# Kernel tuning notes

Hardware: AMD Instinct MI355X
Metric: run time of the kernel (lower is better)

The kernel has to match this reference:

```python
import jax, jax.numpy as jnp
import numpy as np

D = 1024  # input_size == context_size

def setup_inputs() -> dict:
    key = jax.random.key(0)
    ks = jax.random.split(key, 8)
    B, S = 16, 4096
    s = 1.0 / np.sqrt(D)
    return {
        "x": jax.random.normal(ks[0], (B, S, D), dtype=jnp.float32),
        "context": jax.random.normal(ks[1], (B, D), dtype=jnp.float32),
        "W_in": jax.random.uniform(ks[2], (D, D), jnp.float32, -s, s),
        "b_in": jax.random.uniform(ks[3], (D,), jnp.float32, -s, s),
        "W_ctx": jax.random.uniform(ks[4], (D, D), jnp.float32, -s, s),
        "b_ctx": jax.random.uniform(ks[5], (D,), jnp.float32, -s, s),
        "w_att": jax.random.uniform(ks[6], (D,), jnp.float32, -s, s),
        "b_att": jax.random.uniform(ks[7], (), jnp.float32, -s, s),
    }

def reference(x, context, W_in, b_in, W_ctx, b_ctx, w_att, b_att):
    # projected_input: [B,S,D]; projected_context: [B,D] broadcast over S
    pi = jnp.einsum('bsd,ed->bse', x, W_in) + b_in
    pc = jnp.einsum('bd,ed->be', context, W_ctx) + b_ctx
    h = jnp.tanh(pi + pc[:, None, :])                      # [B,S,D]
    scores = jnp.einsum('bsd,d->bs', h, w_att) + b_att      # [B,S]
    weights = jax.nn.softmax(scores, axis=1)                # [B,S]
    context_vector = jnp.einsum('bs,bsd->bd', weights, x)   # [B,D]
    # dropout is identity in eval mode
    return context_vector
```

## Files before the change

kernel.cpp:

```cpp
#include <hip/hip_runtime.h>
#include <hip/hip_bf16.h>
#include <math.h>

#define NB 16
#define NS 4096
#define ND 1024
#define NM (NB * NS)

#define WS_T       0
#define WS_SCORES  16384
#define WS_WEIGHTS (WS_SCORES + NB * NS)
#define WS_SHARED  (WS_WEIGHTS + NB * NS)
#define WS_XBF16   (WS_SHARED + 524288)
#define WS_SPART   (WS_XBF16 + 33554432)
#define WS_NEED    (((size_t)WS_SPART + 524288) * 4)

typedef short v8s __attribute__((ext_vector_type(8)));
typedef float v4f __attribute__((ext_vector_type(4)));
typedef unsigned short ushort;

#define G_AS __attribute__((address_space(1)))
#define L_AS __attribute__((address_space(3)))

__device__ __forceinline__ ushort f2bf(float f) {
    __hip_bfloat16 h = __float2bfloat16(f);
    return *reinterpret_cast<ushort*>(&h);
}

__device__ __forceinline__ float bf2f(ushort u) {
    return __uint_as_float(((unsigned)u) << 16);
}

__device__ __forceinline__ float fast_tanh(float x) {
    float e = __expf(2.0f * x);
    return 1.0f - 2.0f / (e + 1.0f);
}

__global__ __launch_bounds__(256) void convw_kernel(const float* __restrict__ W,
                                                    ushort* __restrict__ Wb) {
    int flat = blockIdx.x * 256 + threadIdx.x;
#pragma unroll
    for (int j = 0; j < 2; ++j) {
        int idx = flat + j * 131072;
        float4 v = ((const float4*)W)[idx];
        ushort4 o;
        o.x = f2bf(v.x); o.y = f2bf(v.y); o.z = f2bf(v.z); o.w = f2bf(v.w);
        ((ushort4*)Wb)[idx] = o;
    }
}

__global__ __launch_bounds__(256) void convx_kernel(const float* __restrict__ x,
                                                    ushort* __restrict__ xb) {
    size_t base = (size_t)blockIdx.x * 256 + threadIdx.x;
#pragma unroll
    for (int i = 0; i < 16; ++i) {
        size_t idx8 = base + (size_t)i * 524288;
        float4 a = ((const float4*)x)[idx8 * 2];
        float4 c = ((const float4*)x)[idx8 * 2 + 1];
        v8s o;
        o[0] = (short)f2bf(a.x); o[1] = (short)f2bf(a.y);
        o[2] = (short)f2bf(a.z); o[3] = (short)f2bf(a.w);
        o[4] = (short)f2bf(c.x); o[5] = (short)f2bf(c.y);
        o[6] = (short)f2bf(c.z); o[7] = (short)f2bf(c.w);
        ((v8s*)xb)[idx8] = o;
    }
}

__global__ __launch_bounds__(256) void tvec_kernel(const float* __restrict__ context,
                                                   const float* __restrict__ W_ctx,
                                                   const float* __restrict__ b_in,
                                                   const float* __restrict__ b_ctx,
                                                   float* __restrict__ t) {
    __shared__ float ctx[ND];
    int b = blockIdx.y;
    int tid = threadIdx.x;
    for (int i = tid; i < ND; i += 256) ctx[i] = context[b * ND + i];
    __syncthreads();
    int e = blockIdx.x * 64 + (tid >> 2);
    int kq = tid & 3;
    const float4* wr = (const float4*)(W_ctx + (size_t)e * ND + kq * 256);
    const float4* cr = (const float4*)(ctx + kq * 256);
    float acc = 0.f;
#pragma unroll 4
    for (int k = 0; k < 64; ++k) {
        float4 w = wr[k];
        float4 c = cr[k];
        acc += c.x * w.x + c.y * w.y + c.z * w.z + c.w * w.w;
    }
    acc += __shfl_xor(acc, 1);
    acc += __shfl_xor(acc, 2);
    if (kq == 0) t[b * ND + e] = acc + b_in[e] + b_ctx[e];
}

__global__ __launch_bounds__(256, 4) void scores_tile_kernel(const ushort* __restrict__ xbf,
                                                             const ushort* __restrict__ Wb,
                                                             const float* __restrict__ t,
                                                             const float* __restrict__ w_att,
                                                             float* __restrict__ spart) {
    __shared__ ushort As[2][4096];
    __shared__ ushort Bs[2][4096];
    __shared__ float red[4][64];

    int tid = threadIdx.x;
    int o = blockIdx.x;
    int rt = (o & 7) * 64 + (o >> 6);
    int ct = (o >> 3) & 7;
    int row0 = rt << 7;
    int e0 = ct << 7;
    int b = row0 >> 12;

    int g0 = tid, g1 = tid + 256;
    const ushort* gaA0 = xbf + (size_t)(row0 + (g0 >> 2)) * ND + (g0 & 3) * 8;
    const ushort* gaA1 = xbf + (size_t)(row0 + (g1 >> 2)) * ND + (g1 & 3) * 8;
    const ushort* gaB0 = Wb  + (size_t)(e0  + (g0 >> 2)) * ND + (g0 & 3) * 8;
    const ushort* gaB1 = Wb  + (size_t)(e0  + (g1 >> 2)) * ND + (g1 & 3) * 8;

    int w = tid >> 6, l = tid & 63;
    int l15 = l & 15, kq4 = l >> 4;
    int R = (w >> 1) * 64;
    int E = (w & 1) * 64;

    v4f acc[4][4];
#pragma unroll
    for (int i = 0; i < 4; ++i)
#pragma unroll
        for (int j = 0; j < 4; ++j) acc[i][j] = (v4f)(0.f);

#define STAGE(BUF, KO)                                                                                              \
    {                                                                                                               \
        __builtin_amdgcn_global_load_lds((const G_AS void*)(gaA0 + (KO)), (L_AS void*)&As[BUF][g0 * 8], 16, 0, 0);  \
        __builtin_amdgcn_global_load_lds((const G_AS void*)(gaA1 + (KO)), (L_AS void*)&As[BUF][g1 * 8], 16, 0, 0);  \
        __builtin_amdgcn_global_load_lds((const G_AS void*)(gaB0 + (KO)), (L_AS void*)&Bs[BUF][g0 * 8], 16, 0, 0);  \
        __builtin_amdgcn_global_load_lds((const G_AS void*)(gaB1 + (KO)), (L_AS void*)&Bs[BUF][g1 * 8], 16, 0, 0);  \
    }

#define COMPUTE(BUF)                                                                          \
    {                                                                                         \
        v8s af[4], bf[4];                                                                     \
        _Pragma("unroll") for (int mf = 0; mf < 4; ++mf)                                      \
            af[mf] = *(const v8s*)&As[BUF][((R + mf * 16 + l15) * 4 + kq4) * 8];              \
        _Pragma("unroll") for (int nf = 0; nf < 4; ++nf)                                      \
            bf[nf] = *(const v8s*)&Bs[BUF][((E + nf * 16 + l15) * 4 + kq4) * 8];              \
        _Pragma("unroll") for (int mf = 0; mf < 4; ++mf)                                      \
            _Pragma("unroll") for (int nf = 0; nf < 4; ++nf)                                  \
                acc[mf][nf] = __builtin_amdgcn_mfma_f32_16x16x32_bf16(af[mf], bf[nf],         \
                                                                      acc[mf][nf], 0, 0, 0);  \
    }

#define KSTEP(KT, BUF, SB, VMTOK, DOST)                              \
    {                                                                \
        __builtin_amdgcn_s_barrier();                                \
        if (DOST) STAGE(SB, ((KT) + 1) * 32);                        \
        asm volatile("s_waitcnt vmcnt(" VMTOK ")" ::: "memory");     \
        __builtin_amdgcn_s_barrier();                                \
        asm volatile("" ::: "memory");                               \
        COMPUTE(BUF);                                                \
    }

    STAGE(0, 0);

    for (int tt = 0; tt < 15; ++tt) {
        KSTEP(2 * tt + 0, 0, 1, "4", true);
        KSTEP(2 * tt + 1, 1, 0, "4", true);
    }
    KSTEP(30, 0, 1, "4", true);
    KSTEP(31, 1, 0, "0", false);

#undef KSTEP
#undef COMPUTE
#undef STAGE

    float s[4][4];
#pragma unroll
    for (int i = 0; i < 4; ++i)
#pragma unroll
        for (int j = 0; j < 4; ++j) s[i][j] = 0.f;

#pragma unroll
    for (int nf = 0; nf < 4; ++nf) {
        int e = e0 + E + nf * 16 + l15;
        float tv = t[b * ND + e];
        float wv = w_att[e];
#pragma unroll
        for (int mf = 0; mf < 4; ++mf)
#pragma unroll
            for (int r = 0; r < 4; ++r)
                s[mf][r] += fast_tanh(acc[mf][nf][r] + tv) * wv;
    }
#pragma unroll
    for (int mf = 0; mf < 4; ++mf)
#pragma unroll
        for (int r = 0; r < 4; ++r) {
            float v = s[mf][r];
            v += __shfl_xor(v, 1);
            v += __shfl_xor(v, 2);
            v += __shfl_xor(v, 4);
            v += __shfl_xor(v, 8);
            s[mf][r] = v;
        }
    if (l15 == 0) {
#pragma unroll
        for (int mf = 0; mf < 4; ++mf)
#pragma unroll
            for (int r = 0; r < 4; ++r)
                red[w][mf * 16 + kq4 * 4 + r] = s[mf][r];
    }
    __syncthreads();
    if (tid < 128) {
        int half = tid >> 6;
        int rl = tid & 63;
        float v = red[half * 2][rl] + red[half * 2 + 1][rl];
        spart[ct * 65536 + row0 + half * 64 + rl] = v;
    }
}

__global__ __launch_bounds__(512) void scores_mfma_kernel(const float* __restrict__ x,
                                                          const ushort* __restrict__ Wb,
                                                          const float* __restrict__ t,
                                                          const float* __restrict__ w_att,
                                                          float* __restrict__ scores) {
    __shared__ ushort As[2][64 * 256];
    __shared__ float red[8][64];

    int tid = threadIdx.x;
    int row0 = blockIdx.x * 64;
    int b = row0 >> 12;
    const float4* xf4 = (const float4*)x;

    int sr = tid >> 3;
    int sc = tid & 7;
    int swzbase = (sr & 7) << 3;

    float4 nx[8];
#pragma unroll
    for (int j = 0; j < 8; ++j)
        nx[j] = xf4[(size_t)(row0 + sr) * 256 + sc + j * 8];
#pragma unroll
    for (int j = 0; j < 8; ++j) {
        int c4 = sc + j * 8;
        ushort4 o;
        o.x = f2bf(nx[j].x); o.y = f2bf(nx[j].y); o.z = f2bf(nx[j].z); o.w = f2bf(nx[j].w);
        *(ushort4*)&As[0][sr * 256 + ((c4 * 4) ^ swzbase)] = o;
    }
    __syncthreads();

    int w = tid >> 6;
    int l = tid & 63;
    int l15 = l & 15;
    int kofs = (l >> 4) * 8;
    int xorv = (l & 7) << 3;
    int n0 = w * 128;

    v4f acc[2][4][4];
#pragma unroll
    for (int p = 0; p < 2; ++p)
#pragma unroll
        for (int i = 0; i < 4; ++i)
#pragma unroll
            for (int j = 0; j < 4; ++j) acc[p][i][j] = (v4f)(0.f);

    const ushort* bbase0 = Wb + (size_t)(n0 + l15) * ND + kofs;
    const ushort* bbase1 = bbase0 + (size_t)64 * ND;

#pragma unroll
    for (int kh = 0; kh < 4; ++kh) {
        if (kh < 3) {
#pragma unroll
            for (int j = 0; j < 8; ++j)
                nx[j] = xf4[(size_t)(row0 + sr) * 256 + (kh + 1) * 64 + sc + j * 8];
        }
        const ushort* Ab = &As[kh & 1][0];
        int kb = kh * 256;

        v8s b0c[4], b0n[4], b1[4];
#pragma unroll
        for (int nf = 0; nf < 4; ++nf) b0c[nf] = *(const v8s*)(bbase0 + (size_t)nf * 16 * ND + kb);

#pragma unroll
        for (int ks = 0; ks < 8; ++ks) {
            int kk = kb + ks * 32;
            int elem = (ks * 32 + kofs) ^ xorv;
            v8s af[4];
#pragma unroll
            for (int mf = 0; mf < 4; ++mf)
                af[mf] = *(const v8s*)&Ab[(mf * 16 + l15) * 256 + elem];
#pragma unroll
            for (int nf = 0; nf < 4; ++nf)
                b1[nf] = *(const v8s*)(bbase1 + (size_t)nf * 16 * ND + kk);
            if (ks < 7) {
#pragma unroll
                for (int nf = 0; nf < 4; ++nf)
                    b0n[nf] = *(const v8s*)(bbase0 + (size_t)nf * 16 * ND + kk + 32);
            }
#pragma unroll
            for (int mf = 0; mf < 4; ++mf)
#pragma unroll
                for (int nf = 0; nf < 4; ++nf)
                    acc[0][mf][nf] = __builtin_amdgcn_mfma_f32_16x16x32_bf16(
                        af[mf], b0c[nf], acc[0][mf][nf], 0, 0, 0);
#pragma unroll
            for (int mf = 0; mf < 4; ++mf)
#pragma unroll
                for (int nf = 0; nf < 4; ++nf)
                    acc[1][mf][nf] = __builtin_amdgcn_mfma_f32_16x16x32_bf16(
                        af[mf], b1[nf], acc[1][mf][nf], 0, 0, 0);
#pragma unroll
            for (int nf = 0; nf < 4; ++nf) b0c[nf] = b0n[nf];
        }

        if (kh < 3) {
#pragma unroll
            for (int j = 0; j < 8; ++j) {
                int c4 = sc + j * 8;
                ushort4 o;
                o.x = f2bf(nx[j].x); o.y = f2bf(nx[j].y); o.z = f2bf(nx[j].z); o.w = f2bf(nx[j].w);
                *(ushort4*)&As[(kh + 1) & 1][sr * 256 + ((c4 * 4) ^ swzbase)] = o;
            }
            __syncthreads();
        }
    }

    float s[4][4];
#pragma unroll
    for (int i = 0; i < 4; ++i)
#pragma unroll
        for (int j = 0; j < 4; ++j) s[i][j] = 0.f;

#pragma unroll
    for (int pass = 0; pass < 2; ++pass)
#pragma unroll
        for (int nf = 0; nf < 4; ++nf) {
            int e = n0 + pass * 64 + nf * 16 + l15;
            float tv = t[b * ND + e];
            float wv = w_att[e];
#pragma unroll
            for (int mf = 0; mf < 4; ++mf)
#pragma unroll
                for (int r = 0; r < 4; ++r)
                    s[mf][r] += fast_tanh(acc[pass][mf][nf][r] + tv) * wv;
        }

#pragma unroll
    for (int mf = 0; mf < 4; ++mf)
#pragma unroll
        for (int r = 0; r < 4; ++r) {
            float v = s[mf][r];
            v += __shfl_xor(v, 1);
            v += __shfl_xor(v, 2);
            v += __shfl_xor(v, 4);
            v += __shfl_xor(v, 8);
            s[mf][r] = v;
        }
    if (l15 == 0) {
#pragma unroll
        for (int mf = 0; mf < 4; ++mf)
#pragma unroll
            for (int r = 0; r < 4; ++r)
                red[w][mf * 16 + (l >> 4) * 4 + r] = s[mf][r];
    }
    __syncthreads();
    if (tid < 64) {
        float v = 0.f;
#pragma unroll
        for (int ww = 0; ww < 8; ++ww) v += red[ww][tid];
        scores[(size_t)b * NS + (row0 & (NS - 1)) + tid] = v;
    }
}

__global__ __launch_bounds__(256) void softmax8_kernel(const float* __restrict__ spart,
                                                       float* __restrict__ weights) {
    int b = blockIdx.x;
    int tid = threadIdx.x;
    float v[16];
    float lmax = -1e30f;
#pragma unroll
    for (int i = 0; i < 16; ++i) {
        int grow = b * NS + tid + i * 256;
        float sum = 0.f;
#pragma unroll
        for (int c = 0; c < 8; ++c) sum += spart[c * 65536 + grow];
        v[i] = sum;
        lmax = fmaxf(lmax, sum);
    }
#pragma unroll
    for (int off = 32; off >= 1; off >>= 1) lmax = fmaxf(lmax, __shfl_xor(lmax, off));
    __shared__ float redm[4];
    int wave = tid >> 6;
    if ((tid & 63) == 0) redm[wave] = lmax;
    __syncthreads();
    float bmax = fmaxf(fmaxf(redm[0], redm[1]), fmaxf(redm[2], redm[3]));

    float lsum = 0.f;
#pragma unroll
    for (int i = 0; i < 16; ++i) {
        v[i] = expf(v[i] - bmax);
        lsum += v[i];
    }
#pragma unroll
    for (int off = 32; off >= 1; off >>= 1) lsum += __shfl_xor(lsum, off);
    __shared__ float reds[4];
    if ((tid & 63) == 0) reds[wave] = lsum;
    __syncthreads();
    float inv = 1.0f / (reds[0] + reds[1] + reds[2] + reds[3]);
#pragma unroll
    for (int i = 0; i < 16; ++i) weights[b * NS + tid + i * 256] = v[i] * inv;
}

__global__ __launch_bounds__(256) void softmax_kernel(const float* __restrict__ scores,
                                                      float* __restrict__ weights) {
    int b = blockIdx.x;
    int tid = threadIdx.x;
    float v[16];
    float lmax = -1e30f;
#pragma unroll
    for (int i = 0; i < 16; ++i) {
        v[i] = scores[b * NS + tid + i * 256];
        lmax = fmaxf(lmax, v[i]);
    }
#pragma unroll
    for (int off = 32; off >= 1; off >>= 1) lmax = fmaxf(lmax, __shfl_xor(lmax, off));
    __shared__ float redm[4];
    int wave = tid >> 6;
    if ((tid & 63) == 0) redm[wave] = lmax;
    __syncthreads();
    float bmax = fmaxf(fmaxf(redm[0], redm[1]), fmaxf(redm[2], redm[3]));

    float lsum = 0.f;
#pragma unroll
    for (int i = 0; i < 16; ++i) {
        v[i] = expf(v[i] - bmax);
        lsum += v[i];
    }
#pragma unroll
    for (int off = 32; off >= 1; off >>= 1) lsum += __shfl_xor(lsum, off);
    __shared__ float reds[4];
    if ((tid & 63) == 0) reds[wave] = lsum;
    __syncthreads();
    float inv = 1.0f / (reds[0] + reds[1] + reds[2] + reds[3]);
#pragma unroll
    for (int i = 0; i < 16; ++i) weights[b * NS + tid + i * 256] = v[i] * inv;
}

__global__ __launch_bounds__(256) void wsum_kernel(const float* __restrict__ x,
                                                   const float* __restrict__ w,
                                                   float* __restrict__ part) {
    int sc = blockIdx.x, b = blockIdx.y;
    int d0 = threadIdx.x * 4;
    const float* xb = x + ((size_t)b * NS + sc * 128) * ND;
    const float* wb = w + b * NS + sc * 128;
    float4 acc = {0.f, 0.f, 0.f, 0.f};
    for (int ss = 0; ss < 128; ++ss) {
        float wv = wb[ss];
        float4 xv = *(const float4*)&xb[(size_t)ss * ND + d0];
        acc.x += wv * xv.x;
        acc.y += wv * xv.y;
        acc.z += wv * xv.z;
        acc.w += wv * xv.w;
    }
    *(float4*)&part[(size_t)(b * 32 + sc) * ND + d0] = acc;
}

__global__ __launch_bounds__(256) void wsum_bf_kernel(const ushort* __restrict__ xbf,
                                                      const float* __restrict__ w,
                                                      float* __restrict__ part) {
    int sc = blockIdx.x, b = blockIdx.y;
    int d0 = threadIdx.x * 4;
    const ushort* xb = xbf + ((size_t)b * NS + sc * 128) * ND;
    const float* wb = w + b * NS + sc * 128;
    float4 acc = {0.f, 0.f, 0.f, 0.f};
    for (int ss = 0; ss < 128; ++ss) {
        float wv = wb[ss];
        ushort4 xv = *(const ushort4*)&xb[(size_t)ss * ND + d0];
        acc.x += wv * bf2f(xv.x);
        acc.y += wv * bf2f(xv.y);
        acc.z += wv * bf2f(xv.z);
        acc.w += wv * bf2f(xv.w);
    }
    *(float4*)&part[(size_t)(b * 32 + sc) * ND + d0] = acc;
}

__global__ __launch_bounds__(256) void reduce_kernel(const float* __restrict__ part,
                                                     float* __restrict__ out) {
    int b = blockIdx.x;
    int d0 = threadIdx.x * 4;
    float4 acc = {0.f, 0.f, 0.f, 0.f};
#pragma unroll
    for (int sc = 0; sc < 32; ++sc) {
        float4 v = *(const float4*)&part[(size_t)(b * 32 + sc) * ND + d0];
        acc.x += v.x;
        acc.y += v.y;
        acc.z += v.z;
        acc.w += v.w;
    }
    *(float4*)&out[b * ND + d0] = acc;
}

extern "C" void kernel_launch(void* const* d_in, const int* in_sizes, int n_in,
                              void* d_out, int out_size, void* d_ws, size_t ws_size,
                              hipStream_t stream) {
    const float* x       = (const float*)d_in[0];
    const float* context = (const float*)d_in[1];
    const float* W_in    = (const float*)d_in[2];
    const float* b_in    = (const float*)d_in[3];
    const float* W_ctx   = (const float*)d_in[4];
    const float* b_ctx   = (const float*)d_in[5];
    const float* w_att   = (const float*)d_in[6];

    float* ws      = (float*)d_ws;
    float* t       = ws + WS_T;
    float* scores  = ws + WS_SCORES;
    float* weights = ws + WS_WEIGHTS;
    ushort* wbf16  = (ushort*)(ws + WS_SHARED);
    ushort* xbf16  = (ushort*)(ws + WS_XBF16);
    float* spart   = ws + WS_SPART;
    float* partfb  = ws + WS_SHARED;
    float* out     = (float*)d_out;

    bool fast = ws_size >= WS_NEED;

    convw_kernel<<<dim3(512), 256, 0, stream>>>(W_in, wbf16);
    tvec_kernel<<<dim3(16, NB), 256, 0, stream>>>(context, W_ctx, b_in, b_ctx, t);
    if (fast) {
        convx_kernel<<<dim3(2048), 256, 0, stream>>>(x, xbf16);
        scores_tile_kernel<<<dim3(4096), 256, 0, stream>>>(xbf16, wbf16, t, w_att, spart);
        softmax8_kernel<<<dim3(NB), 256, 0, stream>>>(spart, weights);
        wsum_bf_kernel<<<dim3(32, NB), 256, 0, stream>>>(xbf16, weights, spart);
        reduce_kernel<<<dim3(NB), 256, 0, stream>>>(spart, out);
    } else {
        scores_mfma_kernel<<<dim3(NM / 64), 512, 0, stream>>>(x, wbf16, t, w_att, scores);
        softmax_kernel<<<dim3(NB), 256, 0, stream>>>(scores, weights);
        wsum_kernel<<<dim3(32, NB), 256, 0, stream>>>(x, weights, partfb);
        reduce_kernel<<<dim3(NB), 256, 0, stream>>>(partfb, out);
    }
}
```

Before: 288.9 us.

## Fuse fp32-to-bf16 conversion of x into the scores GEMM tile loader

Drops the separate pass that converts x to bf16. The scores GEMM now loads fp32 x into registers, converts it and writes bf16 to LDS, while W still streams through direct global-to-LDS loads. The weighted sum reads fp32 x directly, which restores the exact input values there. This removes a full read and write of a 256MB tensor, but the GEMM now reads x at twice the bytes per tile, x is read in fp32 again by the wsum pass, and each k-step adds register staging and conversion work.

```diff
diff --git a/kernel.cpp b/kernel.cpp
--- a/kernel.cpp
+++ b/kernel.cpp
@@ -27,10 +27,6 @@
     return *reinterpret_cast<ushort*>(&h);
 }
 
-__device__ __forceinline__ float bf2f(ushort u) {
-    return __uint_as_float(((unsigned)u) << 16);
-}
-
 __device__ __forceinline__ float fast_tanh(float x) {
     float e = __expf(2.0f * x);
     return 1.0f - 2.0f / (e + 1.0f);
@@ -46,23 +42,6 @@
         ushort4 o;
         o.x = f2bf(v.x); o.y = f2bf(v.y); o.z = f2bf(v.z); o.w = f2bf(v.w);
         ((ushort4*)Wb)[idx] = o;
-    }
-}
-
-__global__ __launch_bounds__(256) void convx_kernel(const float* __restrict__ x,
-                                                    ushort* __restrict__ xb) {
-    size_t base = (size_t)blockIdx.x * 256 + threadIdx.x;
-#pragma unroll
-    for (int i = 0; i < 16; ++i) {
-        size_t idx8 = base + (size_t)i * 524288;
-        float4 a = ((const float4*)x)[idx8 * 2];
-        float4 c = ((const float4*)x)[idx8 * 2 + 1];
-        v8s o;
-        o[0] = (short)f2bf(a.x); o[1] = (short)f2bf(a.y);
-        o[2] = (short)f2bf(a.z); o[3] = (short)f2bf(a.w);
-        o[4] = (short)f2bf(c.x); o[5] = (short)f2bf(c.y);
-        o[6] = (short)f2bf(c.z); o[7] = (short)f2bf(c.w);
-        ((v8s*)xb)[idx8] = o;
     }
 }
 
@@ -92,7 +71,7 @@
     if (kq == 0) t[b * ND + e] = acc + b_in[e] + b_ctx[e];
 }
 
-__global__ __launch_bounds__(256, 4) void scores_tile_kernel(const ushort* __restrict__ xbf,
+__global__ __launch_bounds__(256, 4) void scores_tile_kernel(const float* __restrict__ x,
                                                              const ushort* __restrict__ Wb,
                                                              const float* __restrict__ t,
                                                              const float* __restrict__ w_att,
@@ -110,10 +89,10 @@
     int b = row0 >> 12;
 
     int g0 = tid, g1 = tid + 256;
-    const ushort* gaA0 = xbf + (size_t)(row0 + (g0 >> 2)) * ND + (g0 & 3) * 8;
-    const ushort* gaA1 = xbf + (size_t)(row0 + (g1 >> 2)) * ND + (g1 & 3) * 8;
-    const ushort* gaB0 = Wb  + (size_t)(e0  + (g0 >> 2)) * ND + (g0 & 3) * 8;
-    const ushort* gaB1 = Wb  + (size_t)(e0  + (g1 >> 2)) * ND + (g1 & 3) * 8;
+    const float* gxA0 = x + (size_t)(row0 + (tid >> 2)) * ND + (tid & 3) * 8;
+    const float* gxA1 = gxA0 + (size_t)64 * ND;
+    const ushort* gaB0 = Wb + (size_t)(e0 + (g0 >> 2)) * ND + (g0 & 3) * 8;
+    const ushort* gaB1 = Wb + (size_t)(e0 + (g1 >> 2)) * ND + (g1 & 3) * 8;
 
     int w = tid >> 6, l = tid & 63;
     int l15 = l & 15, kq4 = l >> 4;
@@ -126,12 +105,34 @@
 #pragma unroll
         for (int j = 0; j < 4; ++j) acc[i][j] = (v4f)(0.f);
 
-#define STAGE(BUF, KO)                                                                                              \
-    {                                                                                                               \
-        __builtin_amdgcn_global_load_lds((const G_AS void*)(gaA0 + (KO)), (L_AS void*)&As[BUF][g0 * 8], 16, 0, 0);  \
-        __builtin_amdgcn_global_load_lds((const G_AS void*)(gaA1 + (KO)), (L_AS void*)&As[BUF][g1 * 8], 16, 0, 0);  \
-        __builtin_amdgcn_global_load_lds((const G_AS void*)(gaB0 + (KO)), (L_AS void*)&Bs[BUF][g0 * 8], 16, 0, 0);  \
-        __builtin_amdgcn_global_load_lds((const G_AS void*)(gaB1 + (KO)), (L_AS void*)&Bs[BUF][g1 * 8], 16, 0, 0);  \
+    float4 ra[2][4];
+
+#define ISSUE(KT, RS)                                                                               \
+    {                                                                                               \
+        ra[RS][0] = *(const float4*)(gxA0 + (KT) * 32);                                             \
+        ra[RS][1] = *(const float4*)(gxA0 + (KT) * 32 + 4);                                         \
+        ra[RS][2] = *(const float4*)(gxA1 + (KT) * 32);                                             \
+        ra[RS][3] = *(const float4*)(gxA1 + (KT) * 32 + 4);                                         \
+        __builtin_amdgcn_global_load_lds((const G_AS void*)(gaB0 + (KT) * 32),                      \
+                                         (L_AS void*)&Bs[(KT) & 1][g0 * 8], 16, 0, 0);             \
+        __builtin_amdgcn_global_load_lds((const G_AS void*)(gaB1 + (KT) * 32),                      \
+                                         (L_AS void*)&Bs[(KT) & 1][g1 * 8], 16, 0, 0);             \
+    }
+
+#define WRITEA(RS, BUF)                                                                             \
+    {                                                                                               \
+        v8s w0, w1;                                                                                 \
+        w0[0] = (short)f2bf(ra[RS][0].x); w0[1] = (short)f2bf(ra[RS][0].y);                         \
+        w0[2] = (short)f2bf(ra[RS][0].z); w0[3] = (short)f2bf(ra[RS][0].w);                         \
+        w0[4] = (short)f2bf(ra[RS][1].x); w0[5] = (short)f2bf(ra[RS][1].y);                         \
+        w0[6] = (short)f2bf(ra[RS][1].z); w0[7] = (short)f2bf(ra[RS][1].w);                         \
+        w1[0] = (short)f2bf(ra[RS][2].x); w1[1] = (short)f2bf(ra[RS][2].y);                         \
+        w1[2] = (short)f2bf(ra[RS][2].z); w1[3] = (short)f2bf(ra[RS][2].w);                         \
+        w1[4] = (short)f2bf(ra[RS][3].x); w1[5] = (short)f2bf(ra[RS][3].y);                         \
+        w1[6] = (short)f2bf(ra[RS][3].z); w1[7] = (short)f2bf(ra[RS][3].w);                         \
+        *(v8s*)&As[BUF][g0 * 8] = w0;                                                               \
+        *(v8s*)&As[BUF][g1 * 8] = w1;                                                               \
+        asm volatile("s_waitcnt lgkmcnt(0)" ::: "memory");                                          \
     }
 
 #define COMPUTE(BUF)                                                                          \
@@ -147,28 +148,30 @@
                                                                       acc[mf][nf], 0, 0, 0);  \
     }
 
-#define KSTEP(KT, BUF, SB, VMTOK, DOST)                              \
+#define KSTEP(KT, BUF, CUR, NXT, VMTOK, DOST)                        \
     {                                                                \
         __builtin_amdgcn_s_barrier();                                \
-        if (DOST) STAGE(SB, ((KT) + 1) * 32);                        \
+        if (DOST) ISSUE((KT) + 1, NXT);                              \
         asm volatile("s_waitcnt vmcnt(" VMTOK ")" ::: "memory");     \
+        WRITEA(CUR, BUF);                                            \
         __builtin_amdgcn_s_barrier();                                \
         asm volatile("" ::: "memory");                               \
         COMPUTE(BUF);                                                \
     }
 
-    STAGE(0, 0);
+    ISSUE(0, 0);
 
     for (int tt = 0; tt < 15; ++tt) {
-        KSTEP(2 * tt + 0, 0, 1, "4", true);
-        KSTEP(2 * tt + 1, 1, 0, "4", true);
-    }
-    KSTEP(30, 0, 1, "4", true);
-    KSTEP(31, 1, 0, "0", false);
+        KSTEP(2 * tt + 0, 0, 0, 1, "6", true);
+        KSTEP(2 * tt + 1, 1, 1, 0, "6", true);
+    }
+    KSTEP(30, 0, 0, 1, "6", true);
+    KSTEP(31, 1, 1, 0, "0", false);
 
 #undef KSTEP
 #undef COMPUTE
-#undef STAGE
+#undef WRITEA
+#undef ISSUE
 
     float s[4][4];
 #pragma unroll
@@ -460,25 +463,6 @@
     *(float4*)&part[(size_t)(b * 32 + sc) * ND + d0] = acc;
 }
 
-__global__ __launch_bounds__(256) void wsum_bf_kernel(const ushort* __restrict__ xbf,
-                                                      const float* __restrict__ w,
-                                                      float* __restrict__ part) {
-    int sc = blockIdx.x, b = blockIdx.y;
-    int d0 = threadIdx.x * 4;
-    const ushort* xb = xbf + ((size_t)b * NS + sc * 128) * ND;
-    const float* wb = w + b * NS + sc * 128;
-    float4 acc = {0.f, 0.f, 0.f, 0.f};
-    for (int ss = 0; ss < 128; ++ss) {
-        float wv = wb[ss];
-        ushort4 xv = *(const ushort4*)&xb[(size_t)ss * ND + d0];
-        acc.x += wv * bf2f(xv.x);
-        acc.y += wv * bf2f(xv.y);
-        acc.z += wv * bf2f(xv.z);
-        acc.w += wv * bf2f(xv.w);
-    }
-    *(float4*)&part[(size_t)(b * 32 + sc) * ND + d0] = acc;
-}
-
 __global__ __launch_bounds__(256) void reduce_kernel(const float* __restrict__ part,
                                                      float* __restrict__ out) {
     int b = blockIdx.x;
@@ -511,7 +495,6 @@
     float* scores  = ws + WS_SCORES;
     float* weights = ws + WS_WEIGHTS;
     ushort* wbf16  = (ushort*)(ws + WS_SHARED);
-    ushort* xbf16  = (ushort*)(ws + WS_XBF16);
     float* spart   = ws + WS_SPART;
     float* partfb  = ws + WS_SHARED;
     float* out     = (float*)d_out;
@@ -521,10 +504,9 @@
     convw_kernel<<<dim3(512), 256, 0, stream>>>(W_in, wbf16);
     tvec_kernel<<<dim3(16, NB), 256, 0, stream>>>(context, W_ctx, b_in, b_ctx, t);
     if (fast) {
-        convx_kernel<<<dim3(2048), 256, 0, stream>>>(x, xbf16);
-        scores_tile_kernel<<<dim3(4096), 256, 0, stream>>>(xbf16, wbf16, t, w_att, spart);
+        scores_tile_kernel<<<dim3(4096), 256, 0, stream>>>(x, wbf16, t, w_att, spart);
         softmax8_kernel<<<dim3(NB), 256, 0, stream>>>(spart, weights);
-        wsum_bf_kernel<<<dim3(32, NB), 256, 0, stream>>>(xbf16, weights, spart);
+        wsum_kernel<<<dim3(32, NB), 256, 0, stream>>>(x, weights, spart);
         reduce_kernel<<<dim3(NB), 256, 0, stream>>>(spart, out);
     } else {
         scores_mfma_kernel<<<dim3(NM / 64), 512, 0, stream>>>(x, wbf16, t, w_att, scores);
```

Result: faster. 270.7 us (median of 2 runs) (-6.3%).
